# Kernel optimization log

Hardware: AMD Instinct MI355X
Metric: run time of the kernel (lower is better)

The kernel has to match this reference:

```python
import jax, jax.numpy as jnp
import numpy as np

MASS, CHARGE, ALPHA, BETA = 1.0, 0.5, 0.1, 0.05
ETA = jnp.array([1.0, -1.0, -1.0, -1.0], dtype=jnp.float32)  # Minkowski metric diag


def setup_inputs() -> dict:
    key = jax.random.key(0)
    k1, k2, k3 = jax.random.split(key, 3)
    B = 262144
    y = jax.random.normal(k1, (B, 8), dtype=jnp.float32)
    W = jax.random.normal(k2, (4, 4), dtype=jnp.float32) * 0.3
    V = jax.random.normal(k3, (4, 4), dtype=jnp.float32) * 0.3
    return {"y": y, "W": W, "V": V}


def _lagrangian(z):
    # z = (x, u, A) concatenated, shape [12]
    x, u, A = z[0:4], z[4:8], z[8:12]
    kinetic = 0.5 * MASS * jnp.sum(ETA * u * u)
    coupling = CHARGE * jnp.sum(ETA * u * A)
    xu_term = ALPHA * jnp.sum((x * u) ** 2)      # makes J_xu nontrivial
    uA_term = BETA * jnp.sum(u * A) ** 2          # makes J_Au nontrivial
    return kinetic + coupling + xu_term + uA_term


def reference(y, W, V):
    def A_vec(x):  # vector potential A^mu(x), works on [4] or [B,4]
        return jnp.tanh(x @ W.T) + x @ V.T

    x = y[:, 0:4]   # [B,4] positions
    u = y[:, 4:8]   # [B,4] velocities
    A = A_vec(x)    # [B,4]
    z = jnp.concatenate([x, u, A], axis=1)  # [B,12] = (x,u,A)

    gradL = jax.vmap(jax.grad(_lagrangian))(z)      # [B,12]
    H = jax.vmap(jax.hessian(_lagrangian))(z)       # [B,12,12]

    dL_dx = gradL[:, 0:4]
    dL_dA = gradL[:, 8:12]
    J_xu = H[:, 0:4, 4:8]    # d^2L/(dx^mu du^nu)
    J_uu = H[:, 4:8, 4:8]    # d^2L/(du^mu du^nu)
    J_Au = H[:, 8:12, 4:8]   # d^2L/(dA^mu du^nu)

    # dA_dx[a, nu, i] = dA^i/dx^nu (matches tf.stack(..., axis=2) layout)
    jacA = jax.vmap(jax.jacfwd(A_vec))(x)           # [B, i, nu]
    dA_dx = jnp.transpose(jacA, (0, 2, 1))          # [B, nu, i]

    J_uu_inv = jnp.linalg.pinv(J_uu)                # [B,4,4]

    force = (dL_dx
             + jnp.einsum('ajk,ak->aj', dA_dx, dL_dA)
             - jnp.einsum('ai,aij->aj', u,
                          J_xu + jnp.einsum('ajk,akm->ajm', dA_dx, J_Au)))
    acceleration = jnp.einsum('ai,aij->aj', force, J_uu_inv)  # [B,4]
    return acceleration
```

## Files before the change

kernel.cpp:

```cpp
#include <hip/hip_runtime.h>
#include <math.h>


#define SIX_RCOND 2.86102294921875e-5
#define RCOND     4.76837158203125e-6

__device__ __forceinline__ void model_terms(
    const double* sW, const double* sV,
    const double x[4], const double u[4],
    double A[4], double f[4], double d[4])
{
    const double eta[4] = {1.0, -1.0, -1.0, -1.0};
    const double CHG = 0.5, ALPHA = 0.1, BETA = 0.05;
    double G[4][4];
    #pragma unroll
    for (int j = 0; j < 4; ++j) {
        double t = 0.0, s = 0.0;
        #pragma unroll
        for (int k = 0; k < 4; ++k) { t += sW[j*4+k]*x[k]; s += sV[j*4+k]*x[k]; }
        double th = tanh(t);
        A[j] = th + s;
        double dth = 1.0 - th * th;
        #pragma unroll
        for (int k = 0; k < 4; ++k) G[j][k] = dth * sW[j*4+k] + sV[j*4+k];
    }
    double S = 0.0;
    #pragma unroll
    for (int k = 0; k < 4; ++k) S += u[k] * A[k];
    double P[4], R[4], Q[4];
    #pragma unroll
    for (int j = 0; j < 4; ++j) {
        double p = 0.0, r = 0.0, q = 0.0;
        #pragma unroll
        for (int k = 0; k < 4; ++k) {
            p += G[k][j] * u[k];
            r += G[j][k] * u[k];
            q += G[k][j] * (CHG * eta[k]) * u[k];
        }
        P[j] = p; R[j] = r; Q[j] = q;
    }
    double T = 0.0;
    #pragma unroll
    for (int j = 0; j < 4; ++j) T += u[j] * R[j];
    #pragma unroll
    for (int j = 0; j < 4; ++j) {
        f[j] = -2.0 * ALPHA * x[j] * u[j] * u[j]
             + Q[j]
             + 2.0 * BETA * S * P[j]
             - (CHG * eta[j] + 2.0 * BETA * S) * R[j]
             - 2.0 * BETA * A[j] * T;
        d[j] = eta[j] + 2.0 * ALPHA * x[j] * x[j];
    }
}

__device__ __forceinline__ void sm_solve(
    const double d[4], const double A[4], const double f[4], double acc[4])
{
    const double C2 = 0.1;
    double b[4], fd[4], den = 1.0, w = 0.0;
    #pragma unroll
    for (int j = 0; j < 4; ++j) {
        double inv = 1.0 / d[j];
        b[j]  = A[j] * inv;
        fd[j] = f[j] * inv;
        den  += C2 * A[j] * b[j];
        w    += b[j] * f[j];
    }
    double scale = C2 * w / den;
    #pragma unroll
    for (int j = 0; j < 4; ++j) acc[j] = fd[j] - b[j] * scale;
}

__device__ void jacobi_pinv_solve(
    const double d[4], const double A[4], const double f[4], double acc[4])
{
    const double C2 = 0.1;
    double M[4][4], Vm[4][4];
    #pragma unroll
    for (int r = 0; r < 4; ++r) {
        #pragma unroll
        for (int c = 0; c < 4; ++c) {
            M[r][c] = C2 * A[r] * A[c];
            Vm[r][c] = (r == c) ? 1.0 : 0.0;
        }
        M[r][r] += d[r];
    }
    for (int sweep = 0; sweep < 8; ++sweep) {
        #pragma unroll
        for (int p = 0; p < 3; ++p) {
            #pragma unroll
            for (int q2 = p + 1; q2 < 4; ++q2) {
                double apq = M[p][q2];
                if (fabs(apq) < 1e-280) continue;
                double app = M[p][p], aqq = M[q2][q2];
                double tau = (aqq - app) / (2.0 * apq);
                double tt = ((tau >= 0.0) ? 1.0 : -1.0) /
                            (fabs(tau) + sqrt(1.0 + tau * tau));
                double c = 1.0 / sqrt(1.0 + tt * tt);
                double s = tt * c;
                #pragma unroll
                for (int k = 0; k < 4; ++k) {
                    double mkp = M[k][p], mkq = M[k][q2];
                    M[k][p]  = c * mkp - s * mkq;
                    M[k][q2] = s * mkp + c * mkq;
                }
                #pragma unroll
                for (int k = 0; k < 4; ++k) {
                    double mpk = M[p][k], mqk = M[q2][k];
                    M[p][k]  = c * mpk - s * mqk;
                    M[q2][k] = s * mpk + c * mqk;
                }
                #pragma unroll
                for (int k = 0; k < 4; ++k) {
                    double vkp = Vm[k][p], vkq = Vm[k][q2];
                    Vm[k][p]  = c * vkp - s * vkq;
                    Vm[k][q2] = s * vkp + c * vkq;
                }
            }
        }
    }
    double lam[4], sigmax = 0.0;
    #pragma unroll
    for (int k = 0; k < 4; ++k) {
        lam[k] = M[k][k];
        double a = fabs(lam[k]);
        sigmax = (a > sigmax) ? a : sigmax;
    }
    double cutoff = RCOND * sigmax;
    #pragma unroll
    for (int j = 0; j < 4; ++j) acc[j] = 0.0;
    #pragma unroll
    for (int e = 0; e < 4; ++e) {
        if (fabs(lam[e]) > cutoff) {
            double coef = 0.0;
            #pragma unroll
            for (int k = 0; k < 4; ++k) coef += Vm[k][e] * f[k];
            coef /= lam[e];
            #pragma unroll
            for (int j = 0; j < 4; ++j) acc[j] += coef * Vm[j][e];
        }
    }
}

__global__ __launch_bounds__(256) void fast_kernel(
    const float* __restrict__ y, const float* __restrict__ W,
    const float* __restrict__ V, float* __restrict__ out,
    unsigned int* __restrict__ cnt, int* __restrict__ list,
    unsigned int cap, int B)
{
    __shared__ double sW[16], sV[16];
    if (threadIdx.x < 16)      sW[threadIdx.x]      = (double)W[threadIdx.x];
    else if (threadIdx.x < 32) sV[threadIdx.x - 16] = (double)V[threadIdx.x - 16];
    __syncthreads();

    int i = blockIdx.x * blockDim.x + threadIdx.x;
    if (i >= B) return;

    const float4* y4 = (const float4*)y;
    float4 xv = y4[2 * i];
    float4 uv = y4[2 * i + 1];
    double x[4] = {xv.x, xv.y, xv.z, xv.w};
    double u[4] = {uv.x, uv.y, uv.z, uv.w};

    double A[4], f[4], d[4];
    model_terms(sW, sV, x, u, A, f, d);

    const double C2 = 0.1;
    double mind = 1e300;
    #pragma unroll
    for (int j = 0; j < 4; ++j) {
        double a = fabs(d[j]);
        mind = (a < mind) ? a : mind;
    }
    double p01 = d[0] * d[1], p23 = d[2] * d[3];
    double det = p01 * p23
        + C2 * (A[0]*A[0]*(d[1]*p23) + A[1]*A[1]*(d[0]*p23) +
                A[2]*A[2]*(p01*d[3]) + A[3]*A[3]*(p01*d[2]));
    double sumA2 = 0.0, sumA4 = 0.0, F2 = 0.0;
    #pragma unroll
    for (int j = 0; j < 4; ++j) {
        double Aj2 = A[j] * A[j];
        sumA2 += Aj2; sumA4 += Aj2 * Aj2;
        double Jjj = d[j] + C2 * Aj2;
        F2 += Jjj * Jjj;
    }
    F2 += C2 * C2 * (sumA2 * sumA2 - sumA4);
    double rowmax = 0.0;
    #pragma unroll
    for (int r = 0; r < 4; ++r) {
        double rs = 0.0;
        #pragma unroll
        for (int c = 0; c < 4; ++c) {
            double Jrc = C2 * A[r] * A[c] + ((r == c) ? d[r] : 0.0);
            rs += fabs(Jrc);
        }
        rowmax = (rs > rowmax) ? rs : rowmax;
    }
    double sig_hi2 = rowmax * rowmax;
    sig_hi2 = (F2 < sig_hi2) ? F2 : sig_hi2;
    bool safe = (fabs(det) > SIX_RCOND * sig_hi2 * sig_hi2) && (mind > 1e-3);

    if (safe) {
        double acc[4];
        sm_solve(d, A, f, acc);
        float4 res;
        res.x = (float)acc[0]; res.y = (float)acc[1];
        res.z = (float)acc[2]; res.w = (float)acc[3];
        ((float4*)out)[i] = res;
    } else {
        unsigned int idx = atomicAdd(cnt, 1u);
        if (idx < cap) {
            list[idx] = i;
        } else {
            double acc[4];
            sm_solve(d, A, f, acc);
            float4 res;
            res.x = (float)acc[0]; res.y = (float)acc[1];
            res.z = (float)acc[2]; res.w = (float)acc[3];
            ((float4*)out)[i] = res;
        }
    }
}

__global__ __launch_bounds__(256) void slow_kernel(
    const float* __restrict__ y, const float* __restrict__ W,
    const float* __restrict__ V, float* __restrict__ out,
    const unsigned int* __restrict__ cnt, const int* __restrict__ list,
    unsigned int cap)
{
    __shared__ double sW[16], sV[16];
    if (threadIdx.x < 16)      sW[threadIdx.x]      = (double)W[threadIdx.x];
    else if (threadIdx.x < 32) sV[threadIdx.x - 16] = (double)V[threadIdx.x - 16];
    __syncthreads();

    unsigned int n = *cnt;
    if (n > cap) n = cap;
    int stride = gridDim.x * blockDim.x;
    for (unsigned int j = blockIdx.x * blockDim.x + threadIdx.x; j < n; j += stride) {
        int i = list[j];
        const float4* y4 = (const float4*)y;
        float4 xv = y4[2 * i];
        float4 uv = y4[2 * i + 1];
        double x[4] = {xv.x, xv.y, xv.z, xv.w};
        double u[4] = {uv.x, uv.y, uv.z, uv.w};
        double A[4], f[4], d[4];
        model_terms(sW, sV, x, u, A, f, d);
        double acc[4];
        jacobi_pinv_solve(d, A, f, acc);
        float4 res;
        res.x = (float)acc[0]; res.y = (float)acc[1];
        res.z = (float)acc[2]; res.w = (float)acc[3];
        ((float4*)out)[i] = res;
    }
}

extern "C" void kernel_launch(void* const* d_in, const int* in_sizes, int n_in,
                              void* d_out, int out_size, void* d_ws, size_t ws_size,
                              hipStream_t stream) {
    const float* y = (const float*)d_in[0];
    const float* W = (const float*)d_in[1];
    const float* V = (const float*)d_in[2];
    float* out = (float*)d_out;
    int B = in_sizes[0] / 8;

    unsigned int* cnt = (unsigned int*)d_ws;
    int* list = (int*)((char*)d_ws + 16);
    unsigned int cap = (ws_size > 16) ? (unsigned int)((ws_size - 16) / sizeof(int)) : 0u;
    if (cap > (unsigned int)B) cap = (unsigned int)B;

    hipMemsetAsync(d_ws, 0, 16, stream);

    int block = 256;
    int grid = (B + block - 1) / block;
    fast_kernel<<<grid, block, 0, stream>>>(y, W, V, out, cnt, list, cap, B);
    slow_kernel<<<64, block, 0, stream>>>(y, W, V, out, cnt, list, cap);
}
```

Before: 88.36 us.

## Fuse fast and slow pinv paths into one kernel with per-block shared stash

Merges the two-kernel scheme (fast Sherman-Morrison solve plus a global list of ill-conditioned rows handled by a second kernel) into one kernel. Each block stashes up to 8 unsafe rows' A, f, d in shared memory and solves them with Jacobi after a block barrier. This drops the memset, the second launch, the global atomics and the recomputation of model terms. It also cuts Jacobi sweeps from 8 to 5, which risks less accurate eigenvalues for hard cases, and any overflow beyond 8 per block falls back to the fast solver.

```diff
diff --git a/kernel.cpp b/kernel.cpp
--- a/kernel.cpp
+++ b/kernel.cpp
@@ -4,6 +4,7 @@
 
 #define SIX_RCOND 2.86102294921875e-5
 #define RCOND     4.76837158203125e-6
+#define MAXSLOW   8
 
 __device__ __forceinline__ void model_terms(
     const double* sW, const double* sV,
@@ -85,7 +86,7 @@
         }
         M[r][r] += d[r];
     }
-    for (int sweep = 0; sweep < 8; ++sweep) {
+    for (int sweep = 0; sweep < 5; ++sweep) {
         #pragma unroll
         for (int p = 0; p < 3; ++p) {
             #pragma unroll
@@ -142,115 +143,112 @@
     }
 }
 
-__global__ __launch_bounds__(256) void fast_kernel(
+__global__ __launch_bounds__(256) void rel_particle_kernel(
     const float* __restrict__ y, const float* __restrict__ W,
-    const float* __restrict__ V, float* __restrict__ out,
-    unsigned int* __restrict__ cnt, int* __restrict__ list,
-    unsigned int cap, int B)
+    const float* __restrict__ V, float* __restrict__ out, int B)
 {
     __shared__ double sW[16], sV[16];
-    if (threadIdx.x < 16)      sW[threadIdx.x]      = (double)W[threadIdx.x];
-    else if (threadIdx.x < 32) sV[threadIdx.x - 16] = (double)V[threadIdx.x - 16];
+    __shared__ double stash[MAXSLOW][12];
+    __shared__ int    sidx[MAXSLOW];
+    __shared__ int    scnt;
+
+    int tid = threadIdx.x;
+    if (tid < 16)      sW[tid]      = (double)W[tid];
+    else if (tid < 32) sV[tid - 16] = (double)V[tid - 16];
+    if (tid == 32) scnt = 0;
     __syncthreads();
 
-    int i = blockIdx.x * blockDim.x + threadIdx.x;
-    if (i >= B) return;
-
-    const float4* y4 = (const float4*)y;
-    float4 xv = y4[2 * i];
-    float4 uv = y4[2 * i + 1];
-    double x[4] = {xv.x, xv.y, xv.z, xv.w};
-    double u[4] = {uv.x, uv.y, uv.z, uv.w};
-
-    double A[4], f[4], d[4];
-    model_terms(sW, sV, x, u, A, f, d);
-
-    const double C2 = 0.1;
-    double mind = 1e300;
-    #pragma unroll
-    for (int j = 0; j < 4; ++j) {
-        double a = fabs(d[j]);
-        mind = (a < mind) ? a : mind;
-    }
-    double p01 = d[0] * d[1], p23 = d[2] * d[3];
-    double det = p01 * p23
-        + C2 * (A[0]*A[0]*(d[1]*p23) + A[1]*A[1]*(d[0]*p23) +
-                A[2]*A[2]*(p01*d[3]) + A[3]*A[3]*(p01*d[2]));
-    double sumA2 = 0.0, sumA4 = 0.0, F2 = 0.0;
-    #pragma unroll
-    for (int j = 0; j < 4; ++j) {
-        double Aj2 = A[j] * A[j];
-        sumA2 += Aj2; sumA4 += Aj2 * Aj2;
-        double Jjj = d[j] + C2 * Aj2;
-        F2 += Jjj * Jjj;
-    }
-    F2 += C2 * C2 * (sumA2 * sumA2 - sumA4);
-    double rowmax = 0.0;
-    #pragma unroll
-    for (int r = 0; r < 4; ++r) {
-        double rs = 0.0;
-        #pragma unroll
-        for (int c = 0; c < 4; ++c) {
-            double Jrc = C2 * A[r] * A[c] + ((r == c) ? d[r] : 0.0);
-            rs += fabs(Jrc);
-        }
-        rowmax = (rs > rowmax) ? rs : rowmax;
-    }
-    double sig_hi2 = rowmax * rowmax;
-    sig_hi2 = (F2 < sig_hi2) ? F2 : sig_hi2;
-    bool safe = (fabs(det) > SIX_RCOND * sig_hi2 * sig_hi2) && (mind > 1e-3);
-
-    if (safe) {
-        double acc[4];
-        sm_solve(d, A, f, acc);
-        float4 res;
-        res.x = (float)acc[0]; res.y = (float)acc[1];
-        res.z = (float)acc[2]; res.w = (float)acc[3];
-        ((float4*)out)[i] = res;
-    } else {
-        unsigned int idx = atomicAdd(cnt, 1u);
-        if (idx < cap) {
-            list[idx] = i;
-        } else {
+    int i = blockIdx.x * blockDim.x + tid;
+    if (i < B) {
+        const float4* y4 = (const float4*)y;
+        float4 xv = y4[2 * i];
+        float4 uv = y4[2 * i + 1];
+        double x[4] = {xv.x, xv.y, xv.z, xv.w};
+        double u[4] = {uv.x, uv.y, uv.z, uv.w};
+
+        double A[4], f[4], d[4];
+        model_terms(sW, sV, x, u, A, f, d);
+
+        const double C2 = 0.1;
+        double mind = 1e300;
+        #pragma unroll
+        for (int j = 0; j < 4; ++j) {
+            double a = fabs(d[j]);
+            mind = (a < mind) ? a : mind;
+        }
+        double p01 = d[0] * d[1], p23 = d[2] * d[3];
+        double det = p01 * p23
+            + C2 * (A[0]*A[0]*(d[1]*p23) + A[1]*A[1]*(d[0]*p23) +
+                    A[2]*A[2]*(p01*d[3]) + A[3]*A[3]*(p01*d[2]));
+        double sumA2 = 0.0, sumA4 = 0.0, F2 = 0.0;
+        #pragma unroll
+        for (int j = 0; j < 4; ++j) {
+            double Aj2 = A[j] * A[j];
+            sumA2 += Aj2; sumA4 += Aj2 * Aj2;
+            double Jjj = d[j] + C2 * Aj2;
+            F2 += Jjj * Jjj;
+        }
+        F2 += C2 * C2 * (sumA2 * sumA2 - sumA4);
+        double rowmax = 0.0;
+        #pragma unroll
+        for (int r = 0; r < 4; ++r) {
+            double rs = 0.0;
+            #pragma unroll
+            for (int c = 0; c < 4; ++c) {
+                double Jrc = C2 * A[r] * A[c] + ((r == c) ? d[r] : 0.0);
+                rs += fabs(Jrc);
+            }
+            rowmax = (rs > rowmax) ? rs : rowmax;
+        }
+        double sig_hi2 = rowmax * rowmax;
+        sig_hi2 = (F2 < sig_hi2) ? F2 : sig_hi2;
+        bool safe = (fabs(det) > SIX_RCOND * sig_hi2 * sig_hi2) && (mind > 1e-3);
+
+        if (safe) {
             double acc[4];
             sm_solve(d, A, f, acc);
             float4 res;
             res.x = (float)acc[0]; res.y = (float)acc[1];
             res.z = (float)acc[2]; res.w = (float)acc[3];
             ((float4*)out)[i] = res;
-        }
-    }
-}
-
-__global__ __launch_bounds__(256) void slow_kernel(
-    const float* __restrict__ y, const float* __restrict__ W,
-    const float* __restrict__ V, float* __restrict__ out,
-    const unsigned int* __restrict__ cnt, const int* __restrict__ list,
-    unsigned int cap)
-{
-    __shared__ double sW[16], sV[16];
-    if (threadIdx.x < 16)      sW[threadIdx.x]      = (double)W[threadIdx.x];
-    else if (threadIdx.x < 32) sV[threadIdx.x - 16] = (double)V[threadIdx.x - 16];
+        } else {
+            int k = atomicAdd(&scnt, 1);
+            if (k < MAXSLOW) {
+                sidx[k] = i;
+                #pragma unroll
+                for (int j = 0; j < 4; ++j) {
+                    stash[k][j]     = A[j];
+                    stash[k][4 + j] = f[j];
+                    stash[k][8 + j] = d[j];
+                }
+            } else {
+                double acc[4];
+                sm_solve(d, A, f, acc);
+                float4 res;
+                res.x = (float)acc[0]; res.y = (float)acc[1];
+                res.z = (float)acc[2]; res.w = (float)acc[3];
+                ((float4*)out)[i] = res;
+            }
+        }
+    }
     __syncthreads();
 
-    unsigned int n = *cnt;
-    if (n > cap) n = cap;
-    int stride = gridDim.x * blockDim.x;
-    for (unsigned int j = blockIdx.x * blockDim.x + threadIdx.x; j < n; j += stride) {
-        int i = list[j];
-        const float4* y4 = (const float4*)y;
-        float4 xv = y4[2 * i];
-        float4 uv = y4[2 * i + 1];
-        double x[4] = {xv.x, xv.y, xv.z, xv.w};
-        double u[4] = {uv.x, uv.y, uv.z, uv.w};
+    int n = scnt;
+    if (n > MAXSLOW) n = MAXSLOW;
+    if (tid < n) {
         double A[4], f[4], d[4];
-        model_terms(sW, sV, x, u, A, f, d);
+        #pragma unroll
+        for (int j = 0; j < 4; ++j) {
+            A[j] = stash[tid][j];
+            f[j] = stash[tid][4 + j];
+            d[j] = stash[tid][8 + j];
+        }
         double acc[4];
         jacobi_pinv_solve(d, A, f, acc);
         float4 res;
         res.x = (float)acc[0]; res.y = (float)acc[1];
         res.z = (float)acc[2]; res.w = (float)acc[3];
-        ((float4*)out)[i] = res;
+        ((float4*)out)[sidx[tid]] = res;
     }
 }
 
@@ -262,16 +260,7 @@
     const float* V = (const float*)d_in[2];
     float* out = (float*)d_out;
     int B = in_sizes[0] / 8;
-
-    unsigned int* cnt = (unsigned int*)d_ws;
-    int* list = (int*)((char*)d_ws + 16);
-    unsigned int cap = (ws_size > 16) ? (unsigned int)((ws_size - 16) / sizeof(int)) : 0u;
-    if (cap > (unsigned int)B) cap = (unsigned int)B;
-
-    hipMemsetAsync(d_ws, 0, 16, stream);
-
     int block = 256;
     int grid = (B + block - 1) / block;
-    fast_kernel<<<grid, block, 0, stream>>>(y, W, V, out, cnt, list, cap, B);
-    slow_kernel<<<64, block, 0, stream>>>(y, W, V, out, cnt, list, cap);
-}
+    rel_particle_kernel<<<grid, block, 0, stream>>>(y, W, V, out, B);
+}
```

After: 88.61 us. Within noise of the previous version (+0.3%).
